# Performance work log

Measured on AMD Instinct MI355X. Metric: run time of the kernel, lower is better.

Reference implementation:

```python
import jax, jax.numpy as jnp
import numpy as np

D_IN = 1024
D_OUT = 1024

def setup_inputs() -> dict:
    key = jax.random.key(0)
    ks = jax.random.split(key, 7)
    s = 1.0 / np.sqrt(D_IN)
    x = jax.random.normal(ks[0], (4, 2048, D_IN), dtype=jnp.float32)
    Wq = jax.random.uniform(ks[1], (D_IN, D_OUT), jnp.float32, -s, s)
    Wk = jax.random.uniform(ks[2], (D_IN, D_OUT), jnp.float32, -s, s)
    Wv = jax.random.uniform(ks[3], (D_IN, D_OUT), jnp.float32, -s, s)
    bq = jax.random.uniform(ks[4], (D_OUT,), jnp.float32, -s, s)
    bk = jax.random.uniform(ks[5], (D_OUT,), jnp.float32, -s, s)
    bv = jax.random.uniform(ks[6], (D_OUT,), jnp.float32, -s, s)
    return {"x": x, "Wq": Wq, "Wk": Wk, "Wv": Wv, "bq": bq, "bk": bk, "bv": bv}

def reference(x, Wq, Wk, Wv, bq, bk, bv):
    # x: [b, n, d_in]
    q = jnp.einsum('bnd,de->bne', x, Wq) + bq
    k = jnp.einsum('bnd,de->bne', x, Wk) + bk
    v = jnp.einsum('bnd,de->bne', x, Wv) + bv
    scale = 1.0 / jnp.sqrt(jnp.asarray(k.shape[-1], dtype=x.dtype))
    scores = jnp.einsum('bqe,bke->bqk', q, k) * scale  # [b, n, n]
    weights = jax.nn.softmax(scores, axis=-1)
    return jnp.einsum('bqk,bke->bqe', weights, v)
```

## Files before the change

kernel.cpp:

```cpp
#include <hip/hip_runtime.h>
#include <cstdint>

typedef __bf16 bf16x8 __attribute__((ext_vector_type(8)));
typedef float f32x16 __attribute__((ext_vector_type(16)));

__device__ __forceinline__ unsigned short f2b(float f) {
    union { float f; uint32_t u; } x; x.f = f;
    uint32_t r = (x.u + 0x7fffu + ((x.u >> 16) & 1u)) >> 16;
    return (unsigned short)r;
}
__device__ __forceinline__ float b2f(unsigned short h) {
    union { float f; uint32_t u; } x; x.u = ((uint32_t)h) << 16;
    return x.f;
}

__device__ __forceinline__ long foff(int n, int k, int K) {
    return ((long)(n >> 5) * (K >> 4) + (k >> 4)) * 512 + (((k >> 3) & 1) * 32 + (n & 31)) * 8 + (k & 7);
}

__global__ __launch_bounds__(256) void convert_x_kernel(const float* __restrict__ x,
                                                        unsigned short* __restrict__ xb) {
    int i = (blockIdx.x * 256 + threadIdx.x) * 4;
    float4 v = *(const float4*)(x + i);
    ushort4 o;
    o.x = f2b(v.x); o.y = f2b(v.y); o.z = f2b(v.z); o.w = f2b(v.w);
    *(ushort4*)(xb + i) = o;
}

__global__ __launch_bounds__(1024) void transpose_w_kernel(const float* __restrict__ Wq,
                                                           const float* __restrict__ Wk,
                                                           const float* __restrict__ Wv,
                                                           unsigned short* __restrict__ Wf) {
    __shared__ float tile[32][33];
    const float* W = (blockIdx.z == 0) ? Wq : (blockIdx.z == 1) ? Wk : Wv;
    int n0 = blockIdx.x * 32, k0 = blockIdx.y * 32;
    int tx = threadIdx.x, ty = threadIdx.y;
    tile[ty][tx] = W[(k0 + ty) * 1024 + n0 + tx];
    __syncthreads();
    int n = blockIdx.z * 1024 + n0 + ty;
    int k = k0 + tx;
    Wf[foff(n, k, 1024)] = f2b(tile[tx][ty]);
}

template <int EPI>
__global__ __launch_bounds__(256) void gemm_fs(const unsigned short* __restrict__ A, int lda, long sA,
                                               const unsigned short* __restrict__ Bf, long sB,
                                               void* __restrict__ Cv, long sC, int K,
                                               const float* __restrict__ bq, const float* __restrict__ bk,
                                               const float* __restrict__ bv,
                                               unsigned short* __restrict__ Qb,
                                               unsigned short* __restrict__ Kf,
                                               unsigned short* __restrict__ Vf) {
    __shared__ unsigned short As[2][128 * 64];

    const int tid = threadIdx.x;
    const int wave = tid >> 6, lane = tid & 63;
    const int h = lane >> 5;
    const int l31 = lane & 31;
    const int wm = wave >> 1, wn = wave & 1;
    const long bm = (long)blockIdx.y * 128;
    const long bn = (long)blockIdx.x * 128;

    const unsigned short* Ab = A + (long)blockIdx.z * sA;
    const unsigned short* Bb = Bf + (long)blockIdx.z * sB;

    f32x16 acc[2][2];
#pragma unroll
    for (int mi = 0; mi < 2; ++mi)
#pragma unroll
        for (int ni = 0; ni < 2; ++ni)
#pragma unroll
            for (int r = 0; r < 16; ++r) acc[mi][ni][r] = 0.0f;

    const int srow_in = lane >> 3;
    const int cswz = (lane & 7) ^ srow_in;
    const unsigned short* aptr[4];
    int asloff[4];
#pragma unroll
    for (int j = 0; j < 4; ++j) {
        const int row = j * 32 + wave * 8 + srow_in;
        aptr[j] = Ab + (bm + row) * (long)lda + cswz * 8;
        asloff[j] = (j * 32 + wave * 8) * 64;
    }

    const unsigned short* bptr[2];
#pragma unroll
    for (int ni = 0; ni < 2; ++ni) {
        const long nblk = (bn >> 5) + wn * 2 + ni;
        bptr[ni] = Bb + nblk * (long)(K >> 4) * 512 + lane * 8;
    }

    int aoff[2][4];
#pragma unroll
    for (int mi = 0; mi < 2; ++mi)
#pragma unroll
        for (int kp = 0; kp < 4; ++kp)
            aoff[mi][kp] = (wm * 64 + mi * 32 + l31) * 64 + (((kp * 2 + h) ^ (l31 & 7)) * 8);

    const int nIter = K >> 6;

#pragma unroll
    for (int j = 0; j < 4; ++j)
        __builtin_amdgcn_global_load_lds((const __attribute__((address_space(1))) void*)(aptr[j]),
                                         (__attribute__((address_space(3))) void*)&As[0][asloff[j]], 16, 0, 0);
    __syncthreads();

    for (int it = 0; it < nIter; ++it) {
        const int buf = it & 1;
        if (it + 1 < nIter) {
            const int koff = (it + 1) << 6;
#pragma unroll
            for (int j = 0; j < 4; ++j)
                __builtin_amdgcn_global_load_lds((const __attribute__((address_space(1))) void*)(aptr[j] + koff),
                                                 (__attribute__((address_space(3))) void*)&As[buf ^ 1][asloff[j]], 16, 0, 0);
        }
        bf16x8 bfr[4][2];
#pragma unroll
        for (int kp = 0; kp < 4; ++kp)
#pragma unroll
            for (int ni = 0; ni < 2; ++ni)
                bfr[kp][ni] = *(const bf16x8*)(bptr[ni] + (long)(it * 4 + kp) * 512);
#pragma unroll
        for (int kp = 0; kp < 4; ++kp) {
            bf16x8 af[2];
#pragma unroll
            for (int mi = 0; mi < 2; ++mi)
                af[mi] = *(const bf16x8*)&As[buf][aoff[mi][kp]];
#pragma unroll
            for (int mi = 0; mi < 2; ++mi)
#pragma unroll
                for (int ni = 0; ni < 2; ++ni)
                    acc[mi][ni] = __builtin_amdgcn_mfma_f32_32x32x16_bf16(af[mi], bfr[kp][ni], acc[mi][ni], 0, 0, 0);
        }
        __syncthreads();
    }

#pragma unroll
    for (int mi = 0; mi < 2; ++mi) {
#pragma unroll
        for (int ni = 0; ni < 2; ++ni) {
            const f32x16 a = acc[mi][ni];
            const long col = bn + wn * 64 + ni * 32 + l31;
            const long rowB = bm + wm * 64 + mi * 32 + h * 4;
            if constexpr (EPI == 0) {
                if (col < 1024) {
                    const float bias = bq[col];
#pragma unroll
                    for (int g = 0; g < 4; ++g)
#pragma unroll
                        for (int r = 0; r < 4; ++r)
                            Qb[(rowB + g * 8 + r) * 1024 + col] = f2b((a[g * 4 + r] + bias) * 0.03125f);
                } else if (col < 2048) {
                    const int e = (int)col - 1024;
                    const float bias = bk[e];
                    const long batch = rowB >> 11;
                    const int tokB = (int)(rowB & 2047) & ~31;
                    unsigned short* dst = Kf + batch * (2048L * 1024) +
                                          ((long)(tokB >> 5) * 64 + (e >> 4)) * 512 +
                                          (long)(((e >> 3) & 1) * 32) * 8 + (e & 7);
#pragma unroll
                    for (int g = 0; g < 4; ++g)
#pragma unroll
                        for (int r = 0; r < 4; ++r) {
                            const int tok31 = (int)((rowB + g * 8 + r) & 31);
                            dst[tok31 * 8] = f2b(a[g * 4 + r] + bias);
                        }
                } else {
                    const int e = (int)col - 2048;
                    const float bias = bv[e];
                    const long batch = rowB >> 11;
                    unsigned short* base = Vf + batch * (2048L * 1024) + (long)(e >> 5) * 128 * 512 + l31 * 8;
#pragma unroll
                    for (int g = 0; g < 4; ++g)
#pragma unroll
                        for (int r = 0; r < 4; ++r) {
                            const int tok = (int)((rowB + g * 8 + r) & 2047);
                            base[((long)(tok >> 4)) * 512 + (long)(((tok >> 3) & 1) * 32) * 8 + (tok & 7)] =
                                f2b(a[g * 4 + r] + bias);
                        }
                }
            } else if constexpr (EPI == 1) {
                unsigned short* S = (unsigned short*)Cv + (long)blockIdx.z * sC;
#pragma unroll
                for (int g = 0; g < 4; ++g)
#pragma unroll
                    for (int r = 0; r < 4; ++r)
                        S[(rowB + g * 8 + r) * 2048 + col] = f2b(a[g * 4 + r]);
            } else {
                float* O = (float*)Cv + (long)blockIdx.z * sC;
#pragma unroll
                for (int g = 0; g < 4; ++g)
#pragma unroll
                    for (int r = 0; r < 4; ++r)
                        O[(rowB + g * 8 + r) * 1024 + col] = a[g * 4 + r];
            }
        }
    }
}

__global__ __launch_bounds__(256) void softmax_kernel(unsigned short* __restrict__ S) {
    const long row = blockIdx.x;
    unsigned short* p = S + row * 2048;
    const int tid = threadIdx.x;
    const int wave = tid >> 6, lane = tid & 63;

    ushort4 u0 = *(const ushort4*)&p[tid * 8];
    ushort4 u1 = *(const ushort4*)&p[tid * 8 + 4];
    float v[8];
    v[0] = b2f(u0.x); v[1] = b2f(u0.y); v[2] = b2f(u0.z); v[3] = b2f(u0.w);
    v[4] = b2f(u1.x); v[5] = b2f(u1.y); v[6] = b2f(u1.z); v[7] = b2f(u1.w);

    float m = v[0];
#pragma unroll
    for (int j = 1; j < 8; ++j) m = fmaxf(m, v[j]);
#pragma unroll
    for (int off = 32; off; off >>= 1) m = fmaxf(m, __shfl_xor(m, off, 64));
    __shared__ float redm[4];
    __shared__ float reds[4];
    if (lane == 0) redm[wave] = m;
    __syncthreads();
    m = fmaxf(fmaxf(redm[0], redm[1]), fmaxf(redm[2], redm[3]));

    float s = 0.0f;
#pragma unroll
    for (int j = 0; j < 8; ++j) { v[j] = __expf(v[j] - m); s += v[j]; }
#pragma unroll
    for (int off = 32; off; off >>= 1) s += __shfl_xor(s, off, 64);
    if (lane == 0) reds[wave] = s;
    __syncthreads();
    s = reds[0] + reds[1] + reds[2] + reds[3];
    const float inv = 1.0f / s;

    u0.x = f2b(v[0] * inv); u0.y = f2b(v[1] * inv); u0.z = f2b(v[2] * inv); u0.w = f2b(v[3] * inv);
    u1.x = f2b(v[4] * inv); u1.y = f2b(v[5] * inv); u1.z = f2b(v[6] * inv); u1.w = f2b(v[7] * inv);
    *(ushort4*)&p[tid * 8] = u0;
    *(ushort4*)&p[tid * 8 + 4] = u1;
}

extern "C" void kernel_launch(void* const* d_in, const int* in_sizes, int n_in,
                              void* d_out, int out_size, void* d_ws, size_t ws_size,
                              hipStream_t stream) {
    const float* x  = (const float*)d_in[0];
    const float* Wq = (const float*)d_in[1];
    const float* Wk = (const float*)d_in[2];
    const float* Wv = (const float*)d_in[3];
    const float* bq = (const float*)d_in[4];
    const float* bk = (const float*)d_in[5];
    const float* bv = (const float*)d_in[6];
    float* out = (float*)d_out;

    char* ws = (char*)d_ws;
    unsigned short* xb = (unsigned short*)ws; ws += 8192L * 1024 * 2;
    unsigned short* Wf = (unsigned short*)ws; ws += 3072L * 1024 * 2;
    unsigned short* Qb = (unsigned short*)ws; ws += 8192L * 1024 * 2;
    unsigned short* Kf = (unsigned short*)ws; ws += 8192L * 1024 * 2;
    unsigned short* Vf = (unsigned short*)ws; ws += 8192L * 1024 * 2;
    unsigned short* S  = (unsigned short*)ws; ws += 4L * 2048 * 2048 * 2;

    convert_x_kernel<<<8192, 256, 0, stream>>>(x, xb);
    transpose_w_kernel<<<dim3(32, 32, 3), dim3(32, 32), 0, stream>>>(Wq, Wk, Wv, Wf);
    gemm_fs<0><<<dim3(24, 64, 1), 256, 0, stream>>>(xb, 1024, 0, Wf, 0,
                                                    nullptr, 0, 1024, bq, bk, bv, Qb, Kf, Vf);
    gemm_fs<1><<<dim3(16, 16, 4), 256, 0, stream>>>(Qb, 1024, 2048L * 1024, Kf, 2048L * 1024,
                                                    S, 2048L * 2048, 1024,
                                                    nullptr, nullptr, nullptr, nullptr, nullptr, nullptr);
    softmax_kernel<<<8192, 256, 0, stream>>>(S);
    gemm_fs<2><<<dim3(8, 16, 4), 256, 0, stream>>>(S, 2048, 2048L * 2048, Vf, 2048L * 1024,
                                                   out, 2048L * 1024, 2048,
                                                   nullptr, nullptr, nullptr, nullptr, nullptr, nullptr);
}
```

Baseline: 283.9 us.

## Store all GEMM A operands in fragment layout and drop LDS staging

The x conversion, the Q epilogue and the softmax output now write their data in the MFMA fragment-major layout already used for B operands. The GEMM kernel then loads both A and B fragments straight from global memory into registers with a two-step software prefetch, removing the LDS double buffer and the per-iteration barriers. The cost is more global traffic per block, because A tiles are no longer shared through LDS between waves, plus strided scatter stores in the producer kernels and an extra P buffer.

```diff
diff --git a/kernel.cpp b/kernel.cpp
--- a/kernel.cpp
+++ b/kernel.cpp
@@ -19,12 +19,19 @@
 }
 
 __global__ __launch_bounds__(256) void convert_x_kernel(const float* __restrict__ x,
-                                                        unsigned short* __restrict__ xb) {
-    int i = (blockIdx.x * 256 + threadIdx.x) * 4;
-    float4 v = *(const float4*)(x + i);
-    ushort4 o;
-    o.x = f2b(v.x); o.y = f2b(v.y); o.z = f2b(v.z); o.w = f2b(v.w);
-    *(ushort4*)(xb + i) = o;
+                                                        unsigned short* __restrict__ Xf) {
+    int t = blockIdx.x * 256 + threadIdx.x;
+    int m = t >> 7;
+    int k0 = (t & 127) * 8;
+    const float* p = x + (long)m * 1024 + k0;
+    float4 v0 = *(const float4*)p;
+    float4 v1 = *(const float4*)(p + 4);
+    long off = ((long)(m >> 5) * 64 + (k0 >> 4)) * 512 + (((k0 >> 3) & 1) * 32 + (m & 31)) * 8;
+    ushort4 o0, o1;
+    o0.x = f2b(v0.x); o0.y = f2b(v0.y); o0.z = f2b(v0.z); o0.w = f2b(v0.w);
+    o1.x = f2b(v1.x); o1.y = f2b(v1.y); o1.z = f2b(v1.z); o1.w = f2b(v1.w);
+    *(ushort4*)(Xf + off) = o0;
+    *(ushort4*)(Xf + off + 4) = o1;
 }
 
 __global__ __launch_bounds__(1024) void transpose_w_kernel(const float* __restrict__ Wq,
@@ -43,16 +50,14 @@
 }
 
 template <int EPI>
-__global__ __launch_bounds__(256) void gemm_fs(const unsigned short* __restrict__ A, int lda, long sA,
+__global__ __launch_bounds__(256) void gemm_ff(const unsigned short* __restrict__ Af, long sA,
                                                const unsigned short* __restrict__ Bf, long sB,
                                                void* __restrict__ Cv, long sC, int K,
                                                const float* __restrict__ bq, const float* __restrict__ bk,
                                                const float* __restrict__ bv,
-                                               unsigned short* __restrict__ Qb,
+                                               unsigned short* __restrict__ Qf,
                                                unsigned short* __restrict__ Kf,
                                                unsigned short* __restrict__ Vf) {
-    __shared__ unsigned short As[2][128 * 64];
-
     const int tid = threadIdx.x;
     const int wave = tid >> 6, lane = tid & 63;
     const int h = lane >> 5;
@@ -60,10 +65,19 @@
     const int wm = wave >> 1, wn = wave & 1;
     const long bm = (long)blockIdx.y * 128;
     const long bn = (long)blockIdx.x * 128;
-
-    const unsigned short* Ab = A + (long)blockIdx.z * sA;
+    const int nk = K >> 4;
+
+    const unsigned short* Ab = Af + (long)blockIdx.z * sA;
     const unsigned short* Bb = Bf + (long)blockIdx.z * sB;
 
+    const unsigned short* ap[2];
+    const unsigned short* bp[2];
+#pragma unroll
+    for (int i = 0; i < 2; ++i) {
+        ap[i] = Ab + ((bm >> 5) + wm * 2 + i) * (long)nk * 512 + lane * 8;
+        bp[i] = Bb + ((bn >> 5) + wn * 2 + i) * (long)nk * 512 + lane * 8;
+    }
+
     f32x16 acc[2][2];
 #pragma unroll
     for (int mi = 0; mi < 2; ++mi)
@@ -72,67 +86,38 @@
 #pragma unroll
             for (int r = 0; r < 16; ++r) acc[mi][ni][r] = 0.0f;
 
-    const int srow_in = lane >> 3;
-    const int cswz = (lane & 7) ^ srow_in;
-    const unsigned short* aptr[4];
-    int asloff[4];
-#pragma unroll
-    for (int j = 0; j < 4; ++j) {
-        const int row = j * 32 + wave * 8 + srow_in;
-        aptr[j] = Ab + (bm + row) * (long)lda + cswz * 8;
-        asloff[j] = (j * 32 + wave * 8) * 64;
-    }
-
-    const unsigned short* bptr[2];
-#pragma unroll
-    for (int ni = 0; ni < 2; ++ni) {
-        const long nblk = (bn >> 5) + wn * 2 + ni;
-        bptr[ni] = Bb + nblk * (long)(K >> 4) * 512 + lane * 8;
-    }
-
-    int aoff[2][4];
-#pragma unroll
-    for (int mi = 0; mi < 2; ++mi)
-#pragma unroll
-        for (int kp = 0; kp < 4; ++kp)
-            aoff[mi][kp] = (wm * 64 + mi * 32 + l31) * 64 + (((kp * 2 + h) ^ (l31 & 7)) * 8);
-
-    const int nIter = K >> 6;
-
-#pragma unroll
-    for (int j = 0; j < 4; ++j)
-        __builtin_amdgcn_global_load_lds((const __attribute__((address_space(1))) void*)(aptr[j]),
-                                         (__attribute__((address_space(3))) void*)&As[0][asloff[j]], 16, 0, 0);
-    __syncthreads();
-
-    for (int it = 0; it < nIter; ++it) {
-        const int buf = it & 1;
-        if (it + 1 < nIter) {
-            const int koff = (it + 1) << 6;
-#pragma unroll
-            for (int j = 0; j < 4; ++j)
-                __builtin_amdgcn_global_load_lds((const __attribute__((address_space(1))) void*)(aptr[j] + koff),
-                                                 (__attribute__((address_space(3))) void*)&As[buf ^ 1][asloff[j]], 16, 0, 0);
+    bf16x8 fa[2][2], fb[2][2];
+#pragma unroll
+    for (int s = 0; s < 2; ++s)
+#pragma unroll
+        for (int i = 0; i < 2; ++i) {
+            fa[s][i] = *(const bf16x8*)(ap[i] + (long)s * 512);
+            fb[s][i] = *(const bf16x8*)(bp[i] + (long)s * 512);
         }
-        bf16x8 bfr[4][2];
-#pragma unroll
-        for (int kp = 0; kp < 4; ++kp)
-#pragma unroll
-            for (int ni = 0; ni < 2; ++ni)
-                bfr[kp][ni] = *(const bf16x8*)(bptr[ni] + (long)(it * 4 + kp) * 512);
-#pragma unroll
-        for (int kp = 0; kp < 4; ++kp) {
-            bf16x8 af[2];
+
+#pragma unroll 2
+    for (int ks = 0; ks < nk; ks += 2) {
+        const int kp = (ks + 2 < nk) ? (ks + 2) : 0;
+        bf16x8 na[2][2], nb[2][2];
+#pragma unroll
+        for (int s = 0; s < 2; ++s)
+#pragma unroll
+            for (int i = 0; i < 2; ++i) {
+                na[s][i] = *(const bf16x8*)(ap[i] + (long)(kp + s) * 512);
+                nb[s][i] = *(const bf16x8*)(bp[i] + (long)(kp + s) * 512);
+            }
+#pragma unroll
+        for (int s = 0; s < 2; ++s)
 #pragma unroll
             for (int mi = 0; mi < 2; ++mi)
-                af[mi] = *(const bf16x8*)&As[buf][aoff[mi][kp]];
-#pragma unroll
-            for (int mi = 0; mi < 2; ++mi)
 #pragma unroll
                 for (int ni = 0; ni < 2; ++ni)
-                    acc[mi][ni] = __builtin_amdgcn_mfma_f32_32x32x16_bf16(af[mi], bfr[kp][ni], acc[mi][ni], 0, 0, 0);
-        }
-        __syncthreads();
+                    acc[mi][ni] = __builtin_amdgcn_mfma_f32_32x32x16_bf16(fa[s][mi], fb[s][ni],
+                                                                          acc[mi][ni], 0, 0, 0);
+#pragma unroll
+        for (int s = 0; s < 2; ++s)
+#pragma unroll
+            for (int i = 0; i < 2; ++i) { fa[s][i] = na[s][i]; fb[s][i] = nb[s][i]; }
     }
 
 #pragma unroll
@@ -143,19 +128,15 @@
             const long col = bn + wn * 64 + ni * 32 + l31;
             const long rowB = bm + wm * 64 + mi * 32 + h * 4;
             if constexpr (EPI == 0) {
-                if (col < 1024) {
-                    const float bias = bq[col];
-#pragma unroll
-                    for (int g = 0; g < 4; ++g)
-#pragma unroll
-                        for (int r = 0; r < 4; ++r)
-                            Qb[(rowB + g * 8 + r) * 1024 + col] = f2b((a[g * 4 + r] + bias) * 0.03125f);
-                } else if (col < 2048) {
-                    const int e = (int)col - 1024;
-                    const float bias = bk[e];
-                    const long batch = rowB >> 11;
-                    const int tokB = (int)(rowB & 2047) & ~31;
-                    unsigned short* dst = Kf + batch * (2048L * 1024) +
+                const long batch = rowB >> 11;
+                const int tokB = (int)(rowB & 2047) & ~31;
+                if (col < 2048) {
+                    const bool isQ = (col < 1024);
+                    const int e = (int)(isQ ? col : col - 1024);
+                    const float bias = isQ ? bq[e] : bk[e];
+                    const float scl = isQ ? 0.03125f : 1.0f;
+                    unsigned short* outb = isQ ? Qf : Kf;
+                    unsigned short* dst = outb + batch * (2048L * 1024) +
                                           ((long)(tokB >> 5) * 64 + (e >> 4)) * 512 +
                                           (long)(((e >> 3) & 1) * 32) * 8 + (e & 7);
 #pragma unroll
@@ -163,12 +144,11 @@
 #pragma unroll
                         for (int r = 0; r < 4; ++r) {
                             const int tok31 = (int)((rowB + g * 8 + r) & 31);
-                            dst[tok31 * 8] = f2b(a[g * 4 + r] + bias);
+                            dst[tok31 * 8] = f2b((a[g * 4 + r] + bias) * scl);
                         }
                 } else {
                     const int e = (int)col - 2048;
                     const float bias = bv[e];
-                    const long batch = rowB >> 11;
                     unsigned short* base = Vf + batch * (2048L * 1024) + (long)(e >> 5) * 128 * 512 + l31 * 8;
 #pragma unroll
                     for (int g = 0; g < 4; ++g)
@@ -198,9 +178,10 @@
     }
 }
 
-__global__ __launch_bounds__(256) void softmax_kernel(unsigned short* __restrict__ S) {
+__global__ __launch_bounds__(256) void softmax_kernel(const unsigned short* __restrict__ S,
+                                                      unsigned short* __restrict__ Pf) {
     const long row = blockIdx.x;
-    unsigned short* p = S + row * 2048;
+    const unsigned short* p = S + row * 2048;
     const int tid = threadIdx.x;
     const int wave = tid >> 6, lane = tid & 63;
 
@@ -233,8 +214,13 @@
 
     u0.x = f2b(v[0] * inv); u0.y = f2b(v[1] * inv); u0.z = f2b(v[2] * inv); u0.w = f2b(v[3] * inv);
     u1.x = f2b(v[4] * inv); u1.y = f2b(v[5] * inv); u1.z = f2b(v[6] * inv); u1.w = f2b(v[7] * inv);
-    *(ushort4*)&p[tid * 8] = u0;
-    *(ushort4*)&p[tid * 8 + 4] = u1;
+
+    const long batch = row >> 11;
+    const int r2 = (int)(row & 2047);
+    unsigned short* q = Pf + batch * (2048L * 2048) +
+                        ((long)(r2 >> 5) * 128 + (tid >> 1)) * 512 + ((tid & 1) * 32 + (r2 & 31)) * 8;
+    *(ushort4*)q = u0;
+    *(ushort4*)(q + 4) = u1;
 }
 
 extern "C" void kernel_launch(void* const* d_in, const int* in_sizes, int n_in,
@@ -250,22 +236,23 @@
     float* out = (float*)d_out;
 
     char* ws = (char*)d_ws;
-    unsigned short* xb = (unsigned short*)ws; ws += 8192L * 1024 * 2;
+    unsigned short* Xf = (unsigned short*)ws; ws += 8192L * 1024 * 2;
     unsigned short* Wf = (unsigned short*)ws; ws += 3072L * 1024 * 2;
-    unsigned short* Qb = (unsigned short*)ws; ws += 8192L * 1024 * 2;
+    unsigned short* Qf = (unsigned short*)ws; ws += 8192L * 1024 * 2;
     unsigned short* Kf = (unsigned short*)ws; ws += 8192L * 1024 * 2;
     unsigned short* Vf = (unsigned short*)ws; ws += 8192L * 1024 * 2;
     unsigned short* S  = (unsigned short*)ws; ws += 4L * 2048 * 2048 * 2;
-
-    convert_x_kernel<<<8192, 256, 0, stream>>>(x, xb);
+    unsigned short* Pf = (unsigned short*)ws; ws += 4L * 2048 * 2048 * 2;
+
+    convert_x_kernel<<<4096, 256, 0, stream>>>(x, Xf);
     transpose_w_kernel<<<dim3(32, 32, 3), dim3(32, 32), 0, stream>>>(Wq, Wk, Wv, Wf);
-    gemm_fs<0><<<dim3(24, 64, 1), 256, 0, stream>>>(xb, 1024, 0, Wf, 0,
-                                                    nullptr, 0, 1024, bq, bk, bv, Qb, Kf, Vf);
-    gemm_fs<1><<<dim3(16, 16, 4), 256, 0, stream>>>(Qb, 1024, 2048L * 1024, Kf, 2048L * 1024,
+    gemm_ff<0><<<dim3(24, 64, 1), 256, 0, stream>>>(Xf, 0, Wf, 0,
+                                                    nullptr, 0, 1024, bq, bk, bv, Qf, Kf, Vf);
+    gemm_ff<1><<<dim3(16, 16, 4), 256, 0, stream>>>(Qf, 2048L * 1024, Kf, 2048L * 1024,
                                                     S, 2048L * 2048, 1024,
                                                     nullptr, nullptr, nullptr, nullptr, nullptr, nullptr);
-    softmax_kernel<<<8192, 256, 0, stream>>>(S);
-    gemm_fs<2><<<dim3(8, 16, 4), 256, 0, stream>>>(S, 2048, 2048L * 2048, Vf, 2048L * 1024,
+    softmax_kernel<<<8192, 256, 0, stream>>>(S, Pf);
+    gemm_ff<2><<<dim3(8, 16, 4), 256, 0, stream>>>(Pf, 2048L * 2048, Vf, 2048L * 1024,
                                                    out, 2048L * 1024, 2048,
                                                    nullptr, nullptr, nullptr, nullptr, nullptr, nullptr);
 }
```

New measurement: 321.6 us. +13.3%, slower.
